# Optimization experiments

Measured on AMD Instinct MI355X. Metric: run time of the kernel, lower is better.

The kernel has to match this reference:

```python
import jax, jax.numpy as jnp
import numpy as np

B, T = 8192, 4096

def setup_inputs() -> dict:
    key = jax.random.key(0)
    x = jax.random.randint(key, (B, T, 1), 0, 5).astype(jnp.float32)
    alpha = jnp.full((1, 1), 0.1, dtype=jnp.float32)  # smoothing weight for demand level Z
    beta = jnp.full((1, 1), 0.1, dtype=jnp.float32)   # smoothing weight for demand probability P
    return {"x": x, "alpha": alpha, "beta": beta}


def reference(x, alpha, beta):
    # Faithful translation of the Keras TSBRNN cell stepped over time by RNN().
    # NOTE (faithful to source): the cell unpacks states as (Z, P) but returns
    # them as [P_next, Z_next], so the two states SWAP roles every step.
    # Also faithful: X = inputs[0] uses only the FIRST batch row's value in the
    # level update, while the zero-mask is computed over the full batch.
    batch = x.shape[0]

    def step(carry, x_t):
        Z, P = carry                      # each (B, 1)
        X = x_t[0]                        # (1,) first batch row, as in source
        nz = (x_t != 0).astype(x_t.dtype) # (B, 1) non-zero demand mask
        Z_next = alpha * X + (1.0 - alpha) * Z
        Z_next = Z_next * nz + Z * (1.0 - nz)
        P_next = nz * beta + (1.0 - beta) * P
        out = P_next * Z_next             # TSB forecast = prob * level
        return (P_next, Z_next), out      # swapped order, faithful to source

    Z0 = jnp.zeros((batch, 1), x.dtype)
    P0 = jnp.zeros((batch, 1), x.dtype)
    xs = jnp.swapaxes(x, 0, 1)            # (T, B, 1) time-major for scan
    _, ys = jax.lax.scan(step, (Z0, P0), xs)
    return jnp.swapaxes(ys, 0, 1)         # (B, T, 1) full output sequence
```

## Files before the change

kernel.cpp:

```cpp
#include <hip/hip_runtime.h>


constexpr int T_LEN  = 4096;
constexpr int TILE   = 1024;
constexpr int NTILE  = T_LEN / TILE;
constexpr int CHUNK  = TILE / 64;
constexpr int WPB    = 4;
constexpr int PADREG = TILE + TILE / 16;

__global__ __launch_bounds__(256) void tsb_scan_kernel(
    const float* __restrict__ x,
    const float* __restrict__ alpha_p,
    const float* __restrict__ beta_p,
    float* __restrict__ out,
    int B)
{
    __shared__ float lds[WPB * 2 * PADREG];

    const int tid  = threadIdx.x;
    const int wave = tid >> 6;
    const int lane = tid & 63;
    const int row  = blockIdx.x * WPB + wave;
    if (row >= B) return;

    float* xl = &lds[wave * 2 * PADREG];
    float* Xl = xl + PADREG;

    const float a   = alpha_p[0];
    const float b   = beta_p[0];
    const float oma = 1.0f - a;
    const float omb = 1.0f - b;

    float C1 = 0.f, C2 = 0.f;

    for (int t = 0; t < NTILE; ++t) {
        const float4* xr4 = (const float4*)(x + (size_t)row * T_LEN + t * TILE);
        const float4* Xr4 = (const float4*)(x + t * TILE);

        float xs[16], Xs[16];
#pragma unroll
        for (int i = 0; i < 4; ++i) {
            *(float4*)(xs + 4 * i) = xr4[i * 64 + lane];
            *(float4*)(Xs + 4 * i) = Xr4[i * 64 + lane];
        }
#pragma unroll
        for (int j = 0; j < 16; ++j) {
            int e  = (j >> 2) * 256 + 4 * lane + (j & 3);
            int ap = e + (e >> 4);
            xl[ap] = xs[j];
            Xl[ap] = Xs[j];
        }
        float xc[CHUNK], Xc[CHUNK];
        const int cb = 17 * lane;
#pragma unroll
        for (int j = 0; j < CHUNK; ++j) {
            xc[j] = xl[cb + j];
            Xc[j] = Xl[cb + j];
        }

        float p = 1.f, u = 0.f, q = 1.f, v = 0.f;
#pragma unroll
        for (int h = 0; h < CHUNK / 2; ++h) {
            float x1 = xc[2 * h], x2 = xc[2 * h + 1];
            float X1 = Xc[2 * h], X2 = Xc[2 * h + 1];
            float nz1 = (x1 != 0.f) ? 1.f : 0.f;
            float nz2 = (x2 != 0.f) ? 1.f : 0.f;
            float k1  = (x1 != 0.f) ? oma : 1.f;
            float k2  = (x2 != 0.f) ? oma : 1.f;
            float P = omb * k1;
            float U = omb * a * nz1 * X1 + b * nz2;
            float Q = omb * k2;
            float V = b * k2 * nz1 + a * nz2 * X2;
            u = P * u + U;  p = P * p;
            v = Q * v + V;  q = Q * q;
        }

#pragma unroll
        for (int off = 1; off < 64; off <<= 1) {
            float pi = __shfl_up(p, off, 64);
            float ui = __shfl_up(u, off, 64);
            float qi = __shfl_up(q, off, 64);
            float vi = __shfl_up(v, off, 64);
            if (lane >= off) {
                u = p * ui + u;  p = p * pi;
                v = q * vi + v;  q = q * qi;
            }
        }
        float pp = __shfl_up(p, 1, 64), up = __shfl_up(u, 1, 64);
        float qp = __shfl_up(q, 1, 64), vp = __shfl_up(v, 1, 64);
        float c1 = (lane == 0) ? C1 : (pp * C1 + up);
        float c2 = (lane == 0) ? C2 : (qp * C2 + vp);
        float p63 = __shfl(p, 63, 64), u63 = __shfl(u, 63, 64);
        float q63 = __shfl(q, 63, 64), v63 = __shfl(v, 63, 64);
        float C1n = p63 * C1 + u63;
        float C2n = q63 * C2 + v63;
        C1 = C1n;  C2 = C2n;

#pragma unroll
        for (int j = 0; j < CHUNK; ++j) {
            float xj = xc[j];
            bool  nz = (xj != 0.f);
            float c2n = nz ? (a * Xc[j] + oma * c1) : c1;
            float c1n = (nz ? b : 0.f) + omb * c2;
            c1 = c1n;  c2 = c2n;
            xl[cb + j] = c1 * c2;
        }

        float4* or4 = (float4*)(out + (size_t)row * T_LEN + t * TILE);
#pragma unroll
        for (int i = 0; i < 4; ++i) {
            float os[4];
#pragma unroll
            for (int k = 0; k < 4; ++k) {
                int e = i * 256 + 4 * lane + k;
                os[k] = xl[e + (e >> 4)];
            }
            or4[i * 64 + lane] = *(float4*)os;
        }
    }
}

extern "C" void kernel_launch(void* const* d_in, const int* in_sizes, int n_in,
                              void* d_out, int out_size, void* d_ws, size_t ws_size,
                              hipStream_t stream) {
    const float* x     = (const float*)d_in[0];
    const float* alpha = (const float*)d_in[1];
    const float* beta  = (const float*)d_in[2];
    float* out = (float*)d_out;

    const int B = in_sizes[0] / T_LEN;
    const int blocks = (B + WPB - 1) / WPB;
    tsb_scan_kernel<<<blocks, 64 * WPB, 0, stream>>>(x, alpha, beta, out, B);
}
```

Baseline: 237.5 us.

## Replace LDS transpose with per-lane float4 chunks and prefetch next subtile

```diff
diff --git a/kernel.cpp b/kernel.cpp
--- a/kernel.cpp
+++ b/kernel.cpp
@@ -1,12 +1,10 @@
 #include <hip/hip_runtime.h>
 
 
-constexpr int T_LEN  = 4096;
-constexpr int TILE   = 1024;
-constexpr int NTILE  = T_LEN / TILE;
-constexpr int CHUNK  = TILE / 64;
-constexpr int WPB    = 4;
-constexpr int PADREG = TILE + TILE / 16;
+constexpr int T_LEN = 4096;
+constexpr int SUB   = 256;
+constexpr int NSUB  = T_LEN / SUB;
+constexpr int WPB   = 4;
 
 __global__ __launch_bounds__(256) void tsb_scan_kernel(
     const float* __restrict__ x,
@@ -15,52 +13,37 @@
     float* __restrict__ out,
     int B)
 {
-    __shared__ float lds[WPB * 2 * PADREG];
-
     const int tid  = threadIdx.x;
-    const int wave = tid >> 6;
     const int lane = tid & 63;
-    const int row  = blockIdx.x * WPB + wave;
+    const int row  = blockIdx.x * WPB + (tid >> 6);
     if (row >= B) return;
-
-    float* xl = &lds[wave * 2 * PADREG];
-    float* Xl = xl + PADREG;
 
     const float a   = alpha_p[0];
     const float b   = beta_p[0];
     const float oma = 1.0f - a;
     const float omb = 1.0f - b;
 
+    const float4* xr = (const float4*)(x + (size_t)row * T_LEN);
+    const float4* Xr = (const float4*)x;
+    float4*       orp = (float4*)(out + (size_t)row * T_LEN);
+
     float C1 = 0.f, C2 = 0.f;
 
-    for (int t = 0; t < NTILE; ++t) {
-        const float4* xr4 = (const float4*)(x + (size_t)row * T_LEN + t * TILE);
-        const float4* Xr4 = (const float4*)(x + t * TILE);
+    float4 xn = xr[lane];
+    float4 Xn = Xr[lane];
 
-        float xs[16], Xs[16];
-#pragma unroll
-        for (int i = 0; i < 4; ++i) {
-            *(float4*)(xs + 4 * i) = xr4[i * 64 + lane];
-            *(float4*)(Xs + 4 * i) = Xr4[i * 64 + lane];
+    for (int s = 0; s < NSUB; ++s) {
+        float4 xc4 = xn, Xc4 = Xn;
+        if (s + 1 < NSUB) {
+            xn = xr[(s + 1) * 64 + lane];
+            Xn = Xr[(s + 1) * 64 + lane];
         }
-#pragma unroll
-        for (int j = 0; j < 16; ++j) {
-            int e  = (j >> 2) * 256 + 4 * lane + (j & 3);
-            int ap = e + (e >> 4);
-            xl[ap] = xs[j];
-            Xl[ap] = Xs[j];
-        }
-        float xc[CHUNK], Xc[CHUNK];
-        const int cb = 17 * lane;
-#pragma unroll
-        for (int j = 0; j < CHUNK; ++j) {
-            xc[j] = xl[cb + j];
-            Xc[j] = Xl[cb + j];
-        }
+        const float* xc = (const float*)&xc4;
+        const float* Xc = (const float*)&Xc4;
 
         float p = 1.f, u = 0.f, q = 1.f, v = 0.f;
 #pragma unroll
-        for (int h = 0; h < CHUNK / 2; ++h) {
+        for (int h = 0; h < 2; ++h) {
             float x1 = xc[2 * h], x2 = xc[2 * h + 1];
             float X1 = Xc[2 * h], X2 = Xc[2 * h + 1];
             float nz1 = (x1 != 0.f) ? 1.f : 0.f;
@@ -92,31 +75,20 @@
         float c2 = (lane == 0) ? C2 : (qp * C2 + vp);
         float p63 = __shfl(p, 63, 64), u63 = __shfl(u, 63, 64);
         float q63 = __shfl(q, 63, 64), v63 = __shfl(v, 63, 64);
-        float C1n = p63 * C1 + u63;
-        float C2n = q63 * C2 + v63;
-        C1 = C1n;  C2 = C2n;
+        float nC1 = p63 * C1 + u63;
+        float nC2 = q63 * C2 + v63;
+        C1 = nC1;  C2 = nC2;
 
+        float os[4];
 #pragma unroll
-        for (int j = 0; j < CHUNK; ++j) {
-            float xj = xc[j];
-            bool  nz = (xj != 0.f);
+        for (int j = 0; j < 4; ++j) {
+            bool  nz  = (xc[j] != 0.f);
             float c2n = nz ? (a * Xc[j] + oma * c1) : c1;
             float c1n = (nz ? b : 0.f) + omb * c2;
             c1 = c1n;  c2 = c2n;
-            xl[cb + j] = c1 * c2;
+            os[j] = c1 * c2;
         }
-
-        float4* or4 = (float4*)(out + (size_t)row * T_LEN + t * TILE);
-#pragma unroll
-        for (int i = 0; i < 4; ++i) {
-            float os[4];
-#pragma unroll
-            for (int k = 0; k < 4; ++k) {
-                int e = i * 256 + 4 * lane + k;
-                os[k] = xl[e + (e >> 4)];
-            }
-            or4[i * 64 + lane] = *(float4*)os;
-        }
+        orp[s * 64 + lane] = *(const float4*)os;
     }
 }
 
```

New measurement: 242.7 us. +2.2%, slower.
